# Performance work log

Hardware: AMD Instinct MI355X
Metric: run time of the kernel (lower is better)

The kernel has to match this reference:

```python
import jax, jax.numpy as jnp
import numpy as np

CELLS = 56
EPS = 1e-9

def setup_inputs() -> dict:
    key = jax.random.key(0)
    k1, k2 = jax.random.split(key)
    B = 512
    F = CELLS * CELLS * 15  # 47040 floats per sample
    output = jax.random.uniform(k1, (B, F), dtype=jnp.float32)
    target = jax.random.uniform(k2, (B, F), dtype=jnp.float32)
    return {"output": output, "target": target}

def reference(output, target):
    B = output.shape[0]
    # reshape flat vector into [B, cells^2, 15] slots: x,y,w,h,conf,classes[5:14]
    o = output.reshape(B, CELLS * CELLS, 15)
    t = target.reshape(B, CELLS * CELLS, 15)
    # coordinate loss: only x (slice [i*15 : i*15+1]) plus sqrt(w)/sqrt(h) terms
    coord = (o[..., 0] - t[..., 0]) ** 2 \
          + (jnp.sqrt(o[..., 2]) - jnp.sqrt(t[..., 2])) ** 2 \
          + (jnp.sqrt(o[..., 3]) - jnp.sqrt(t[..., 3])) ** 2
    # binary cross-entropy on confidence (slot 4)
    conf = -(t[..., 4] * jnp.log(o[..., 4] + EPS)
             + (1.0 - t[..., 4]) * jnp.log(1.0 - o[..., 4] + EPS))
    # class loss: sum of squared diffs over slots 5:14 (9 elements)
    cls = jnp.sum((t[..., 5:14] - o[..., 5:14]) ** 2, axis=-1)
    # cell is counted only if output x-coordinate is nonzero (torch.is_nonzero gate)
    mask = o[..., 0] != 0
    per_cell = jnp.where(mask, coord + conf + cls, 0.0)
    return jnp.sum(per_cell)
```

## Files before the change

kernel.cpp:

```cpp
#include <hip/hip_runtime.h>


constexpr int CPT = 256;
constexpr int TF  = CPT * 15;
#define EPSF 1e-9f

__global__ __launch_bounds__(256) void yolo_loss_kernel(
    const float* __restrict__ o, const float* __restrict__ t,
    float* __restrict__ out_sum, int n_cells)
{
    __shared__ __align__(16) float so[TF];
    __shared__ __align__(16) float st[TF];
    __shared__ float wsum[4];

    const int tid = threadIdx.x;
    const int n_tiles = (n_cells + CPT - 1) / CPT;
    const long lim4 = ((long)n_cells * 15) / 4;
    const float4* o4 = (const float4*)o;
    const float4* t4 = (const float4*)t;

    float acc = 0.f;

    for (int tile = blockIdx.x; tile < n_tiles; tile += gridDim.x) {
        __syncthreads();
        const long b4 = (long)tile * (TF / 4);
        #pragma unroll
        for (int i = tid; i < TF / 4; i += 256) {
            long g = b4 + i;
            if (g < lim4) {
                ((float4*)so)[i] = o4[g];
                ((float4*)st)[i] = t4[g];
            }
        }
        __syncthreads();

        const int cell = tile * CPT + tid;
        if (cell < n_cells) {
            const float* oc = so + tid * 15;
            const float* tc = st + tid * 15;
            const float o0 = oc[0];
            if (o0 != 0.f) {
                const float d0 = o0 - tc[0];
                const float dw = sqrtf(oc[2]) - sqrtf(tc[2]);
                const float dh = sqrtf(oc[3]) - sqrtf(tc[3]);
                const float tv = tc[4], ov = oc[4];
                const float conf = -(tv * __logf(ov + EPSF)
                                   + (1.f - tv) * __logf(1.f - ov + EPSF));
                float s = d0 * d0 + dw * dw + dh * dh + conf;
                #pragma unroll
                for (int k = 5; k < 14; ++k) {
                    const float d = tc[k] - oc[k];
                    s += d * d;
                }
                acc += s;
            }
        }
    }

    #pragma unroll
    for (int off = 32; off; off >>= 1) acc += __shfl_down(acc, off, 64);
    if ((tid & 63) == 0) wsum[tid >> 6] = acc;
    __syncthreads();
    if (tid == 0) atomicAdd(out_sum, wsum[0] + wsum[1] + wsum[2] + wsum[3]);
}

extern "C" void kernel_launch(void* const* d_in, const int* in_sizes, int n_in,
                              void* d_out, int out_size, void* d_ws, size_t ws_size,
                              hipStream_t stream) {
    const float* o = (const float*)d_in[0];
    const float* t = (const float*)d_in[1];
    float* out = (float*)d_out;
    const int n = in_sizes[0];
    const int n_cells = n / 15;

    hipMemsetAsync(out, 0, sizeof(float), stream);

    const int grid = 1024;
    yolo_loss_kernel<<<grid, 256, 0, stream>>>(o, t, out, n_cells);
}
```

Measured before the change: 207.4 us.

## Replace LDS-staged tiles with register quad-of-cells loads and lane shuffles

Drops the shared-memory staging and its barriers. Each group of 15 lanes now loads one float4 per lane covering four cells (60 floats), with a software-prefetched next iteration. The per-cell gate comes from lane shuffles and per-lane slot-role masks precomputed once. It also rewrites the sqrt difference as a+b-2*sqrt(ab), uses log2-based BCE, and raises the grid to 1792. One lane in 16 sits idle, and a generic fallback kernel handles sizes not divisible by 60.

```diff
diff --git a/kernel.cpp b/kernel.cpp
--- a/kernel.cpp
+++ b/kernel.cpp
@@ -1,64 +1,126 @@
 #include <hip/hip_runtime.h>
 
 
-constexpr int CPT = 256;
-constexpr int TF  = CPT * 15;
 #define EPSF 1e-9f
+#define LN2F 0.69314718055994530942f
 
-__global__ __launch_bounds__(256) void yolo_loss_kernel(
+__global__ __launch_bounds__(256) void yolo_loss_quad(
     const float* __restrict__ o, const float* __restrict__ t,
-    float* __restrict__ out_sum, int n_cells)
+    float* __restrict__ out_sum, unsigned n_quads, unsigned n_steps)
 {
-    __shared__ __align__(16) float so[TF];
-    __shared__ __align__(16) float st[TF];
-    __shared__ float wsum[4];
+    const int tid  = threadIdx.x;
+    const int lane = tid & 63;
+    const unsigned r    = (unsigned)tid & 15u;
+    const bool     r_ok = r < 15u;
+    const int      gsel = lane & 48;
 
-    const int tid = threadIdx.x;
-    const int n_tiles = (n_cells + CPT - 1) / CPT;
-    const long lim4 = ((long)n_cells * 15) / 4;
+    bool b_sq[4], b_z[4], b_b4[4], c_lo[4], c_hi[4];
+    #pragma unroll
+    for (int j = 0; j < 4; ++j) {
+        const unsigned e = r * 4u + (unsigned)j;
+        const unsigned c = e / 15u;
+        const unsigned s = e - c * 15u;
+        b_sq[j] = (s == 2u) | (s == 3u);
+        b_z [j] = (s == 1u) | (s == 14u);
+        b_b4[j] = (s == 4u);
+        c_lo[j] = (c & 1u) != 0u;
+        c_hi[j] = (c & 2u) != 0u;
+    }
+
+    const unsigned quads_per_step = (gridDim.x * 256u) >> 4;
+    unsigned q = blockIdx.x * 16u + ((unsigned)tid >> 4);
+
     const float4* o4 = (const float4*)o;
     const float4* t4 = (const float4*)t;
 
     float acc = 0.f;
 
-    for (int tile = blockIdx.x; tile < n_tiles; tile += gridDim.x) {
-        __syncthreads();
-        const long b4 = (long)tile * (TF / 4);
+    float4 co = make_float4(1.f, 1.f, 1.f, 1.f), ct = co;
+    bool cur_ok = r_ok && (q < n_quads);
+    if (cur_ok) { const unsigned fi = q * 15u + r; co = o4[fi]; ct = t4[fi]; }
+
+    for (unsigned step = 1; step <= n_steps; ++step) {
+        float4 no = make_float4(1.f, 1.f, 1.f, 1.f), nt = no;
+        const unsigned qn = q + quads_per_step;
+        const bool nxt_ok = (step < n_steps) && r_ok && (qn < n_quads);
+        if (nxt_ok) { const unsigned fi = qn * 15u + r; no = o4[fi]; nt = t4[fi]; }
+
+        const float g0 = __shfl(co.x, gsel + 0,  64);
+        const float g1 = __shfl(co.w, gsel + 3,  64);
+        const float g2 = __shfl(co.z, gsel + 7,  64);
+        const float g3 = __shfl(co.y, gsel + 11, 64);
+
+        const float oe[4] = {co.x, co.y, co.z, co.w};
+        const float te[4] = {ct.x, ct.y, ct.z, ct.w};
+
+        float ob4 = oe[3], tb4 = te[3];
         #pragma unroll
-        for (int i = tid; i < TF / 4; i += 256) {
-            long g = b4 + i;
-            if (g < lim4) {
-                ((float4*)so)[i] = o4[g];
-                ((float4*)st)[i] = t4[g];
-            }
+        for (int j = 2; j >= 0; --j) {
+            ob4 = b_b4[j] ? oe[j] : ob4;
+            tb4 = b_b4[j] ? te[j] : tb4;
         }
-        __syncthreads();
+        const float l1  = __log2f(ob4 + EPSF);
+        const float l2  = __log2f((1.f - ob4) + EPSF);
+        const float bce = -LN2F * (tb4 * l1 + (1.f - tb4) * l2);
 
-        const int cell = tile * CPT + tid;
-        if (cell < n_cells) {
-            const float* oc = so + tid * 15;
-            const float* tc = st + tid * 15;
-            const float o0 = oc[0];
-            if (o0 != 0.f) {
-                const float d0 = o0 - tc[0];
-                const float dw = sqrtf(oc[2]) - sqrtf(tc[2]);
-                const float dh = sqrtf(oc[3]) - sqrtf(tc[3]);
-                const float tv = tc[4], ov = oc[4];
-                const float conf = -(tv * __logf(ov + EPSF)
-                                   + (1.f - tv) * __logf(1.f - ov + EPSF));
-                float s = d0 * d0 + dw * dw + dh * dh + conf;
-                #pragma unroll
-                for (int k = 5; k < 14; ++k) {
-                    const float d = tc[k] - oc[k];
-                    s += d * d;
-                }
-                acc += s;
-            }
+        float s_iter = 0.f;
+        #pragma unroll
+        for (int j = 0; j < 4; ++j) {
+            const float gate = c_hi[j] ? (c_lo[j] ? g3 : g2)
+                                       : (c_lo[j] ? g1 : g0);
+            const float ox = oe[j], tx = te[j];
+            const float d  = ox - tx;
+            float v = d * d;
+            const float s23 = (ox + tx) - 2.f * __builtin_amdgcn_sqrtf(ox * tx);
+            v = b_sq[j] ? s23 : v;
+            v = b_b4[j] ? bce : v;
+            v = b_z [j] ? 0.f : v;
+            v = (gate != 0.f) ? v : 0.f;
+            s_iter += v;
         }
+        acc += cur_ok ? s_iter : 0.f;
+
+        co = no; ct = nt; cur_ok = nxt_ok; q = qn;
     }
 
     #pragma unroll
     for (int off = 32; off; off >>= 1) acc += __shfl_down(acc, off, 64);
+    __shared__ float wsum[4];
+    if ((tid & 63) == 0) wsum[tid >> 6] = acc;
+    __syncthreads();
+    if (tid == 0) atomicAdd(out_sum, wsum[0] + wsum[1] + wsum[2] + wsum[3]);
+}
+
+__device__ __forceinline__ float bce_of(float ox, float tx) {
+    const float l1 = __log2f(ox + EPSF);
+    const float l2 = __log2f((1.f - ox) + EPSF);
+    return -LN2F * (tx * l1 + (1.f - tx) * l2);
+}
+
+__global__ __launch_bounds__(256) void yolo_loss_generic(
+    const float* __restrict__ o, const float* __restrict__ t,
+    float* __restrict__ out_sum, int n_cells)
+{
+    const int tid = threadIdx.x;
+    const int stride = gridDim.x * 256;
+    float acc = 0.f;
+    for (int c = blockIdx.x * 256 + tid; c < n_cells; c += stride) {
+        const float* oc = o + (size_t)c * 15;
+        const float* tc = t + (size_t)c * 15;
+        const float o0 = oc[0];
+        if (o0 != 0.f) {
+            const float d0 = o0 - tc[0];
+            const float w2 = oc[2] + tc[2] - 2.f * __builtin_amdgcn_sqrtf(oc[2] * tc[2]);
+            const float h2 = oc[3] + tc[3] - 2.f * __builtin_amdgcn_sqrtf(oc[3] * tc[3]);
+            float s = d0 * d0 + w2 + h2 + bce_of(oc[4], tc[4]);
+            #pragma unroll
+            for (int k = 5; k < 14; ++k) { const float d = tc[k] - oc[k]; s += d * d; }
+            acc += s;
+        }
+    }
+    #pragma unroll
+    for (int off = 32; off; off >>= 1) acc += __shfl_down(acc, off, 64);
+    __shared__ float wsum[4];
     if ((tid & 63) == 0) wsum[tid >> 6] = acc;
     __syncthreads();
     if (tid == 0) atomicAdd(out_sum, wsum[0] + wsum[1] + wsum[2] + wsum[3]);
@@ -71,10 +133,16 @@
     const float* t = (const float*)d_in[1];
     float* out = (float*)d_out;
     const int n = in_sizes[0];
-    const int n_cells = n / 15;
 
     hipMemsetAsync(out, 0, sizeof(float), stream);
 
-    const int grid = 1024;
-    yolo_loss_kernel<<<grid, 256, 0, stream>>>(o, t, out, n_cells);
+    if (n % 60 == 0) {
+        const unsigned n_quads = (unsigned)(n / 60);
+        unsigned grid = 1792;
+        const unsigned qps = grid * 16u;
+        const unsigned n_steps = (n_quads + qps - 1u) / qps;
+        yolo_loss_quad<<<grid, 256, 0, stream>>>(o, t, out, n_quads, n_steps);
+    } else {
+        yolo_loss_generic<<<1792, 256, 0, stream>>>(o, t, out, n / 15);
+    }
 }
```

Result: slower. 211.5 us (+2.0%).
